# Optimization experiments

Hardware: AMD Instinct MI355X
Metric: run time of the kernel (lower is better)

Reference implementation:

```python
import jax, jax.numpy as jnp
import numpy as np


def setup_inputs() -> dict:
    key = jax.random.key(0)
    ks = jax.random.split(key, 9)
    N_POI, N_TIME, D = 10000, 48, 500
    S, L = 2048, 4096  # state_len (cur), seq_len (his)
    return {
        "his": jax.random.randint(ks[0], (L,), 0, N_POI, dtype=jnp.int32),
        "cur": jax.random.randint(ks[1], (S,), 0, N_POI, dtype=jnp.int32),
        "his_t": jax.random.randint(ks[2], (L,), 0, N_TIME, dtype=jnp.int32),
        "cur_t": jax.random.randint(ks[3], (S,), 0, N_TIME, dtype=jnp.int32),
        "poi_distance_mat": jax.random.uniform(ks[4], (N_POI, N_POI), dtype=jnp.float32),
        "time_sim_mat": jax.random.uniform(ks[5], (N_TIME, N_TIME), dtype=jnp.float32),
        "user_emb": jax.random.normal(ks[6], (S, D), dtype=jnp.float32),
        "id_emb": jax.random.normal(ks[7], (L, D), dtype=jnp.float32),
        "socail_uid_emb": jax.random.normal(ks[8], (D,), dtype=jnp.float32),
        "w1_socail": jnp.float32(0.6),
        "w2_socail": jnp.float32(0.4),
    }


def reference(his, cur, his_t, cur_t, poi_distance_mat, time_sim_mat,
              user_emb, id_emb, socail_uid_emb, w1_socail, w2_socail):
    # Attn_loc: energies[i,j] = 1/dist[cur[i],his[j]] if nonzero else 1e-6
    d = poi_distance_mat[cur[:, None], his[None, :]]          # [S, L] gather
    nz = d != 0
    loc_energy = jnp.where(nz, 1.0 / jnp.where(nz, d, 1.0), 1e-6)
    attn_loc = jax.nn.softmax(loc_energy, axis=-1)

    # Attn_time: energies[i,j] = time_sim[cur_t[i], his_t[j]]
    time_energy = time_sim_mat[cur_t[:, None], his_t[None, :]]  # [S, L]
    attn_time = jax.nn.softmax(time_energy, axis=-1)

    # Attn_user ('dot'): w1 * <user_emb[i], id_emb[j]> + w2 * <socail, id_emb[j]>
    user_energy = (w1_socail * jnp.einsum('sd,ld->sl', user_emb, id_emb)
                   + w2_socail * (id_emb @ socail_uid_emb)[None, :])  # [S, L]
    attn_user = jax.nn.softmax(user_energy, axis=-1)

    return jnp.stack([attn_loc, attn_time, attn_user])  # [3, S, L]
```

## Files before the change

### kernel.cpp

```cpp
#include <hip/hip_runtime.h>
#include <math.h>

#define S_DIM 2048
#define L_DIM 4096
#define D_DIM 500
#define NPOI 10000
#define NTIME 48
#define EXP_SHIFT 40.0f

typedef __attribute__((ext_vector_type(8))) short short8;
typedef __attribute__((ext_vector_type(16))) float f32x16;

#define A_BYTES 4194304
#define PLANE_BYTES 12582912
#define LDSBUF 49152

__device__ __forceinline__ float wave_max(float v) {
#pragma unroll
  for (int o = 32; o > 0; o >>= 1) v = fmaxf(v, __shfl_down(v, o, 64));
  return v;
}
__device__ __forceinline__ float wave_sum(float v) {
#pragma unroll
  for (int o = 32; o > 0; o >>= 1) v += __shfl_down(v, o, 64);
  return v;
}
__device__ __forceinline__ float half_sum(float v) {
#pragma unroll
  for (int o = 16; o > 0; o >>= 1) v += __shfl_xor(v, o, 64);
  return v;
}
__device__ __forceinline__ short f2bf(float x) {
  union { float f; unsigned u; } v;
  v.f = x;
  const unsigned r = v.u + 0x7fffu + ((v.u >> 16) & 1u);
  return (short)(r >> 16);
}
__device__ __forceinline__ float bf2f(short h) {
  union { unsigned u; float f; } v;
  v.u = ((unsigned)(unsigned short)h) << 16;
  return v.f;
}

__global__ __launch_bounds__(256) void split_table_kernel(
    const float* __restrict__ U, const float* __restrict__ Id,
    const float* __restrict__ w1p, const float* __restrict__ soc,
    const float* __restrict__ w2p, const int* __restrict__ his_t,
    const float* __restrict__ T, short* __restrict__ planes,
    float* __restrict__ bias, float* __restrict__ P) {
  const int tid = threadIdx.x;
  if (blockIdx.x == gridDim.x - 1) {
    __shared__ int cnt[NTIME];
    __shared__ float Ts[NTIME * NTIME];
    if (tid < NTIME) cnt[tid] = 0;
    __syncthreads();
    for (int l = tid; l < L_DIM; l += 256) atomicAdd(&cnt[his_t[l]], 1);
    for (int i = tid; i < NTIME * NTIME; i += 256) Ts[i] = T[i];
    __syncthreads();
    if (tid < NTIME) {
      float m = -1e30f;
      for (int t = 0; t < NTIME; ++t) m = fmaxf(m, Ts[tid * NTIME + t]);
      float den = 0.f;
      for (int t = 0; t < NTIME; ++t)
        den += (float)cnt[t] * __expf(Ts[tid * NTIME + t] - m);
      const float inv = 1.0f / den;
      for (int t = 0; t < NTIME; ++t)
        P[tid * NTIME + t] = __expf(Ts[tid * NTIME + t] - m) * inv;
    }
    return;
  }
  const int chunk = blockIdx.x * 256 + tid;
  const int row = chunk >> 6;
  const int lq = chunk & 63;
  const bool isA = row < S_DIM;
  const float scale = isA ? w1p[0] : 1.0f;
  const float* src = isA ? (U + (size_t)row * D_DIM)
                         : (Id + (size_t)(row - S_DIM) * D_DIM);
  const int k0 = lq * 8;
  float dot = 0.f;
  short h[8], l[8];
#pragma unroll
  for (int e = 0; e < 8; ++e) {
    const int k = k0 + e;
    const float v = (k < D_DIM) ? src[k] : 0.0f;
    if (!isA && k < D_DIM) dot += v * soc[k];
    const float x = scale * v;
    const short hb = f2bf(x);
    h[e] = hb;
    l[e] = f2bf(x - bf2f(hb));
  }
  const int ks = lq >> 2, g = lq & 3;
  if (isA) {
    const int mb = row >> 8, rin = row & 255;
    const int gs = g ^ (rin & 3) ^ ((rin >> 2) & 3);
    char* base =
        (char*)planes + (size_t)(mb * 16 + ks) * 32768 + rin * 64 + gs * 16;
    *reinterpret_cast<int4*>(base) = *reinterpret_cast<const int4*>(h);
    *reinterpret_cast<int4*>(base + 16384) = *reinterpret_cast<const int4*>(l);
  } else {
    const int rb = row - S_DIM;
    const int nb = rb >> 7, rin = rb & 127;
    const int gs = g ^ (rin & 3) ^ ((rin >> 2) & 3);
    char* base = (char*)planes + A_BYTES + (size_t)(nb * 16 + ks) * 16384 +
                 rin * 64 + gs * 16;
    *reinterpret_cast<int4*>(base) = *reinterpret_cast<const int4*>(h);
    *reinterpret_cast<int4*>(base + 8192) = *reinterpret_cast<const int4*>(l);
    const float d = wave_sum(dot);
    if ((tid & 63) == 0) bias[rb] = w2p[0] * d;
  }
}

__global__ __launch_bounds__(512, 2) void user_gemm_mfma(
    const short* __restrict__ planes, const float* __restrict__ bias,
    float* __restrict__ part, float* __restrict__ outX) {
  __shared__ __attribute__((aligned(1024))) char lds[2 * LDSBUF];
  const int tid = threadIdx.x;
  const int lane = tid & 63;
  const int wid = tid >> 6;
  const int ob = (blockIdx.x & 7) * 32 + (blockIdx.x >> 3);
  const int nb = ob >> 3;
  const int mb = ob & 7;
  const int bm = mb * 256, bn = nb * 128;
  const char* gA = (const char*)planes + (size_t)mb * 16 * 32768;
  const char* gB = (const char*)planes + A_BYTES + (size_t)nb * 16 * 16384;
  const int wm = (wid >> 1) * 64;
  const int wn = (wid & 1) * 64;
  const int r32 = lane & 31;
  const int khl = lane >> 5;

  f32x16 acc[2][2] = {};

#define STAGE(ks_, buf_)                                                      \
  {                                                                           \
    const int _ks = (ks_);                                                    \
    char* _dst = lds + (buf_)*LDSBUF;                                         \
    _Pragma("unroll") for (int q = 0; q < 6; ++q) {                           \
      const int off = (q * 512 + tid) * 16;                                   \
      if (q < 4) {                                                            \
        __builtin_amdgcn_global_load_lds(                                     \
            (const __attribute__((address_space(1))) unsigned*)(gA +          \
                (size_t)_ks * 32768 + off),                                   \
            (__attribute__((address_space(3))) unsigned*)(_dst + off), 16, 0, \
            0);                                                               \
      } else {                                                                \
        __builtin_amdgcn_global_load_lds(                                     \
            (const __attribute__((address_space(1))) unsigned*)(gB +          \
                (size_t)_ks * 16384 + (off - 32768)),                         \
            (__attribute__((address_space(3))) unsigned*)(_dst + off), 16, 0, \
            0);                                                               \
      }                                                                       \
    }                                                                         \
  }

  STAGE(0, 0);
  __syncthreads();
  int buf = 0;
  for (int ks = 0; ks < 16; ++ks) {
    if (ks < 15) STAGE(ks + 1, buf ^ 1);
    const char* La = lds + buf * LDSBUF;
    const char* Lb = La + 32768;
#pragma unroll
    for (int s16 = 0; s16 < 2; ++s16) {
      short8 ah[2], al[2], bh[2], bl[2];
#pragma unroll
      for (int i = 0; i < 2; ++i) {
        const int ra = wm + i * 32 + r32;
        const int ga = ((s16 * 2 + khl) ^ (ra & 3) ^ ((ra >> 2) & 3)) * 16;
        ah[i] = *reinterpret_cast<const short8*>(La + ra * 64 + ga);
        al[i] = *reinterpret_cast<const short8*>(La + 16384 + ra * 64 + ga);
        const int rbb = wn + i * 32 + r32;
        const int gb = ((s16 * 2 + khl) ^ (rbb & 3) ^ ((rbb >> 2) & 3)) * 16;
        bh[i] = *reinterpret_cast<const short8*>(Lb + rbb * 64 + gb);
        bl[i] = *reinterpret_cast<const short8*>(Lb + 8192 + rbb * 64 + gb);
      }
#pragma unroll
      for (int i = 0; i < 2; ++i)
#pragma unroll
        for (int j = 0; j < 2; ++j) {
          acc[i][j] = __builtin_amdgcn_mfma_f32_32x32x16_bf16(
              ah[i], bh[j], acc[i][j], 0, 0, 0);
          acc[i][j] = __builtin_amdgcn_mfma_f32_32x32x16_bf16(
              ah[i], bl[j], acc[i][j], 0, 0, 0);
          acc[i][j] = __builtin_amdgcn_mfma_f32_32x32x16_bf16(
              al[i], bh[j], acc[i][j], 0, 0, 0);
        }
    }
    __syncthreads();
    buf ^= 1;
  }
#undef STAGE

  const int slot = nb * 2 + (wn >> 6);
  float bj[2];
#pragma unroll
  for (int j = 0; j < 2; ++j) bj[j] = bias[bn + wn + j * 32 + r32];
#pragma unroll
  for (int i = 0; i < 2; ++i) {
#pragma unroll
    for (int reg = 0; reg < 16; ++reg) {
      const int rowm = bm + wm + i * 32 + 4 * khl + (reg & 3) + 8 * (reg >> 2);
      const float e0 = __expf(acc[i][0][reg] + bj[0] - EXP_SHIFT);
      const float e1 = __expf(acc[i][1][reg] + bj[1] - EXP_SHIFT);
      outX[(size_t)rowm * L_DIM + bn + wn + r32] = e0;
      outX[(size_t)rowm * L_DIM + bn + wn + 32 + r32] = e1;
      const float hs = half_sum(e0 + e1);
      if (r32 == 0) part[(size_t)rowm * 64 + slot] = hs;
    }
  }
}

__global__ __launch_bounds__(256) void finalize_kernel(
    const int* __restrict__ cur, const int* __restrict__ his,
    const float* __restrict__ poi, const int* __restrict__ cur_t,
    const int* __restrict__ his_t, const float* __restrict__ P,
    const float* __restrict__ part, float* __restrict__ out_loc,
    float* __restrict__ out_time, float* __restrict__ out_user) {
  __shared__ __attribute__((aligned(16))) float rowbuf[NPOI];
  __shared__ float Prow[NTIME];
  __shared__ float redm[4];
  __shared__ float reds[4];
  __shared__ float sinv_sh;
  const int s = blockIdx.x;
  const int tid = threadIdx.x;
  if (tid < NTIME) Prow[tid] = P[cur_t[s] * NTIME + tid];
  if (tid < 64) {
    float p = part[(size_t)s * 64 + tid];
    p = wave_sum(p);
    if (tid == 0) sinv_sh = 1.0f / p;
  }
  const float* row = poi + (size_t)cur[s] * NPOI;
  for (int i = tid; i < NPOI / 4; i += 256)
    *reinterpret_cast<float4*>(&rowbuf[i * 4]) =
        *reinterpret_cast<const float4*>(row + i * 4);
  __syncthreads();
  const float sinv = sinv_sh;
  float* ou = out_user + (size_t)s * L_DIM;
#pragma unroll
  for (int q = 0; q < 4; ++q) {
    float4 x = *reinterpret_cast<const float4*>(&ou[(q * 256 + tid) * 4]);
    x.x *= sinv; x.y *= sinv; x.z *= sinv; x.w *= sinv;
    *reinterpret_cast<float4*>(&ou[(q * 256 + tid) * 4]) = x;
  }
  float v[16];
  float lmax = -1e30f;
#pragma unroll
  for (int j = 0; j < 16; ++j) {
    const int l = j * 256 + tid;
    const float d = rowbuf[his[l]];
    const float e = (d != 0.0f) ? (1.0f / d) : 1e-6f;
    v[j] = e;
    lmax = fmaxf(lmax, e);
  }
  lmax = wave_max(lmax);
  if ((tid & 63) == 0) redm[tid >> 6] = lmax;
  __syncthreads();
  const float m = fmaxf(fmaxf(redm[0], redm[1]), fmaxf(redm[2], redm[3]));
  float lsum = 0.f;
#pragma unroll
  for (int j = 0; j < 16; ++j) {
    v[j] = __expf(v[j] - m);
    lsum += v[j];
  }
  lsum = wave_sum(lsum);
  if ((tid & 63) == 0) reds[tid >> 6] = lsum;
  __syncthreads();
  const float inv = 1.0f / (reds[0] + reds[1] + reds[2] + reds[3]);
  float* ol = out_loc + (size_t)s * L_DIM;
  float* ot = out_time + (size_t)s * L_DIM;
#pragma unroll
  for (int j = 0; j < 16; ++j) {
    const int l = j * 256 + tid;
    ol[l] = v[j] * inv;
    ot[l] = Prow[his_t[l]];
  }
}

extern "C" void kernel_launch(void* const* d_in, const int* in_sizes, int n_in,
                              void* d_out, int out_size, void* d_ws,
                              size_t ws_size, hipStream_t stream) {
  const int* his = (const int*)d_in[0];
  const int* cur = (const int*)d_in[1];
  const int* his_t = (const int*)d_in[2];
  const int* cur_t = (const int*)d_in[3];
  const float* poi = (const float*)d_in[4];
  const float* tsim = (const float*)d_in[5];
  const float* uemb = (const float*)d_in[6];
  const float* idemb = (const float*)d_in[7];
  const float* soc = (const float*)d_in[8];
  const float* w1 = (const float*)d_in[9];
  const float* w2 = (const float*)d_in[10];

  float* out = (float*)d_out;
  float* out_loc = out;
  float* out_time = out + (size_t)S_DIM * L_DIM;
  float* out_user = out + 2 * (size_t)S_DIM * L_DIM;

  const size_t aux_bytes = (size_t)(L_DIM + NTIME * NTIME + S_DIM * 64) * 4;
  short* planes;
  float* bias;
  if (ws_size >= PLANE_BYTES + aux_bytes) {
    planes = (short*)d_ws;
    bias = (float*)((char*)d_ws + PLANE_BYTES);
  } else {
    planes = (short*)out_loc;
    bias = (float*)d_ws;
  }
  float* P = bias + L_DIM;
  float* part = P + NTIME * NTIME;

  hipLaunchKernelGGL(split_table_kernel,
                     dim3((S_DIM + L_DIM) * 64 / 256 + 1), dim3(256), 0,
                     stream, uemb, idemb, w1, soc, w2, his_t, tsim, planes,
                     bias, P);
  hipLaunchKernelGGL(user_gemm_mfma, dim3(256), dim3(512), 0, stream, planes,
                     bias, part, out_user);
  hipLaunchKernelGGL(finalize_kernel, dim3(S_DIM), dim3(256), 0, stream, cur,
                     his, poi, cur_t, his_t, P, part, out_loc, out_time,
                     out_user);
}
```

Baseline: 88.60 us.

## Store exp scores as packed bf16 intermediate and halve GEMM block tile

The GEMM kernel now writes its exponentiated user scores as packed bf16 pairs into a workspace buffer instead of fp32 into the output. The finalize kernel then unpacks them, normalizes and writes fp32, so the intermediate round-trip traffic is halved. The GEMM block tile also shrinks from 256x128 to 128x128 with 256 threads and 512 blocks, which uses less LDS and gives more blocks. This adds bf16 rounding of the unnormalized exponentials, and it only takes effect if the workspace is large enough.

```diff
diff --git a/kernel.cpp b/kernel.cpp
--- a/kernel.cpp
+++ b/kernel.cpp
@@ -13,7 +13,7 @@
 
 #define A_BYTES 4194304
 #define PLANE_BYTES 12582912
-#define LDSBUF 49152
+#define LDSBUF 32768
 
 __device__ __forceinline__ float wave_max(float v) {
 #pragma unroll
@@ -110,19 +110,22 @@
   }
 }
 
-__global__ __launch_bounds__(512, 2) void user_gemm_mfma(
+__global__ __launch_bounds__(256, 2) void user_gemm_mfma(
     const short* __restrict__ planes, const float* __restrict__ bias,
-    float* __restrict__ part, float* __restrict__ outX) {
+    float* __restrict__ part, unsigned* __restrict__ Xp,
+    float* __restrict__ outX) {
   __shared__ __attribute__((aligned(1024))) char lds[2 * LDSBUF];
   const int tid = threadIdx.x;
   const int lane = tid & 63;
   const int wid = tid >> 6;
-  const int ob = (blockIdx.x & 7) * 32 + (blockIdx.x >> 3);
-  const int nb = ob >> 3;
-  const int mb = ob & 7;
-  const int bm = mb * 256, bn = nb * 128;
-  const char* gA = (const char*)planes + (size_t)mb * 16 * 32768;
+  const int ob = (blockIdx.x & 7) * 64 + (blockIdx.x >> 3);
+  const int nb = ob >> 4;
+  const int mbb = ob & 15;
+  const int mb256 = mbb >> 1, hh = mbb & 1;
+  const int bm = mbb * 128, bn = nb * 128;
+  const char* gA = (const char*)planes + (size_t)mb256 * 16 * 32768;
   const char* gB = (const char*)planes + A_BYTES + (size_t)nb * 16 * 16384;
+  const int h8 = hh * 8192;
   const int wm = (wid >> 1) * 64;
   const int wn = (wid & 1) * 64;
   const int r32 = lane & 31;
@@ -132,23 +135,18 @@
 
 #define STAGE(ks_, buf_)                                                      \
   {                                                                           \
-    const int _ks = (ks_);                                                    \
+    const char* gAk = gA + (size_t)(ks_)*32768 + h8;                          \
+    const char* gBk = gB + (size_t)(ks_)*16384;                               \
     char* _dst = lds + (buf_)*LDSBUF;                                         \
-    _Pragma("unroll") for (int q = 0; q < 6; ++q) {                           \
-      const int off = (q * 512 + tid) * 16;                                   \
-      if (q < 4) {                                                            \
-        __builtin_amdgcn_global_load_lds(                                     \
-            (const __attribute__((address_space(1))) unsigned*)(gA +          \
-                (size_t)_ks * 32768 + off),                                   \
-            (__attribute__((address_space(3))) unsigned*)(_dst + off), 16, 0, \
-            0);                                                               \
-      } else {                                                                \
-        __builtin_amdgcn_global_load_lds(                                     \
-            (const __attribute__((address_space(1))) unsigned*)(gB +          \
-                (size_t)_ks * 16384 + (off - 32768)),                         \
-            (__attribute__((address_space(3))) unsigned*)(_dst + off), 16, 0, \
-            0);                                                               \
-      }                                                                       \
+    _Pragma("unroll") for (int q = 0; q < 8; ++q) {                           \
+      const int off = (q * 256 + tid) * 16;                                   \
+      const char* src = (q < 2)   ? (gAk + off)                               \
+                        : (q < 4) ? (gAk + off + 8192)                        \
+                                  : (gBk + off - 16384);                      \
+      __builtin_amdgcn_global_load_lds(                                       \
+          (const __attribute__((address_space(1))) unsigned*)src,             \
+          (__attribute__((address_space(3))) unsigned*)(_dst + off), 16, 0,   \
+          0);                                                                 \
     }                                                                         \
   }
 
@@ -158,7 +156,7 @@
   for (int ks = 0; ks < 16; ++ks) {
     if (ks < 15) STAGE(ks + 1, buf ^ 1);
     const char* La = lds + buf * LDSBUF;
-    const char* Lb = La + 32768;
+    const char* Lb = La + 16384;
 #pragma unroll
     for (int s16 = 0; s16 < 2; ++s16) {
       short8 ah[2], al[2], bh[2], bl[2];
@@ -167,7 +165,7 @@
         const int ra = wm + i * 32 + r32;
         const int ga = ((s16 * 2 + khl) ^ (ra & 3) ^ ((ra >> 2) & 3)) * 16;
         ah[i] = *reinterpret_cast<const short8*>(La + ra * 64 + ga);
-        al[i] = *reinterpret_cast<const short8*>(La + 16384 + ra * 64 + ga);
+        al[i] = *reinterpret_cast<const short8*>(La + 8192 + ra * 64 + ga);
         const int rbb = wn + i * 32 + r32;
         const int gb = ((s16 * 2 + khl) ^ (rbb & 3) ^ ((rbb >> 2) & 3)) * 16;
         bh[i] = *reinterpret_cast<const short8*>(Lb + rbb * 64 + gb);
@@ -201,8 +199,14 @@
       const int rowm = bm + wm + i * 32 + 4 * khl + (reg & 3) + 8 * (reg >> 2);
       const float e0 = __expf(acc[i][0][reg] + bj[0] - EXP_SHIFT);
       const float e1 = __expf(acc[i][1][reg] + bj[1] - EXP_SHIFT);
-      outX[(size_t)rowm * L_DIM + bn + wn + r32] = e0;
-      outX[(size_t)rowm * L_DIM + bn + wn + 32 + r32] = e1;
+      if (Xp) {
+        const unsigned u = ((unsigned)(unsigned short)f2bf(e0)) |
+                           (((unsigned)(unsigned short)f2bf(e1)) << 16);
+        Xp[(size_t)rowm * 2048 + ((bn + wn) >> 1) + r32] = u;
+      } else {
+        outX[(size_t)rowm * L_DIM + bn + wn + r32] = e0;
+        outX[(size_t)rowm * L_DIM + bn + wn + 32 + r32] = e1;
+      }
       const float hs = half_sum(e0 + e1);
       if (r32 == 0) part[(size_t)rowm * 64 + slot] = hs;
     }
@@ -213,8 +217,9 @@
     const int* __restrict__ cur, const int* __restrict__ his,
     const float* __restrict__ poi, const int* __restrict__ cur_t,
     const int* __restrict__ his_t, const float* __restrict__ P,
-    const float* __restrict__ part, float* __restrict__ out_loc,
-    float* __restrict__ out_time, float* __restrict__ out_user) {
+    const float* __restrict__ part, const unsigned* __restrict__ Xp,
+    float* __restrict__ out_loc, float* __restrict__ out_time,
+    float* __restrict__ out_user) {
   __shared__ __attribute__((aligned(16))) float rowbuf[NPOI];
   __shared__ float Prow[NTIME];
   __shared__ float redm[4];
@@ -235,11 +240,26 @@
   __syncthreads();
   const float sinv = sinv_sh;
   float* ou = out_user + (size_t)s * L_DIM;
-#pragma unroll
-  for (int q = 0; q < 4; ++q) {
-    float4 x = *reinterpret_cast<const float4*>(&ou[(q * 256 + tid) * 4]);
-    x.x *= sinv; x.y *= sinv; x.z *= sinv; x.w *= sinv;
-    *reinterpret_cast<float4*>(&ou[(q * 256 + tid) * 4]) = x;
+  if (Xp) {
+    const unsigned* xr = Xp + (size_t)s * 2048;
+#pragma unroll
+    for (int qq = 0; qq < 8; ++qq) {
+      const int q = qq * 256 + tid;
+      const unsigned u = xr[q];
+      const int g = (q >> 5) << 6, r = q & 31;
+      union { unsigned uu; float f; } a, b;
+      a.uu = u << 16;
+      b.uu = u & 0xffff0000u;
+      ou[g + r] = a.f * sinv;
+      ou[g + r + 32] = b.f * sinv;
+    }
+  } else {
+#pragma unroll
+    for (int q = 0; q < 4; ++q) {
+      float4 x = *reinterpret_cast<const float4*>(&ou[(q * 256 + tid) * 4]);
+      x.x *= sinv; x.y *= sinv; x.z *= sinv; x.w *= sinv;
+      *reinterpret_cast<float4*>(&ou[(q * 256 + tid) * 4]) = x;
+    }
   }
   float v[16];
   float lmax = -1e30f;
@@ -295,10 +315,16 @@
   float* out_time = out + (size_t)S_DIM * L_DIM;
   float* out_user = out + 2 * (size_t)S_DIM * L_DIM;
 
-  const size_t aux_bytes = (size_t)(L_DIM + NTIME * NTIME + S_DIM * 64) * 4;
+  const size_t base_aux = (size_t)(L_DIM + NTIME * NTIME + S_DIM * 64) * 4;
+  const size_t xp_bytes = (size_t)S_DIM * 2048 * 4;
   short* planes;
   float* bias;
-  if (ws_size >= PLANE_BYTES + aux_bytes) {
+  unsigned* Xp = nullptr;
+  if (ws_size >= PLANE_BYTES + base_aux + xp_bytes) {
+    planes = (short*)d_ws;
+    bias = (float*)((char*)d_ws + PLANE_BYTES);
+    Xp = (unsigned*)((char*)d_ws + PLANE_BYTES + base_aux);
+  } else if (ws_size >= PLANE_BYTES + base_aux) {
     planes = (short*)d_ws;
     bias = (float*)((char*)d_ws + PLANE_BYTES);
   } else {
@@ -312,9 +338,9 @@
                      dim3((S_DIM + L_DIM) * 64 / 256 + 1), dim3(256), 0,
                      stream, uemb, idemb, w1, soc, w2, his_t, tsim, planes,
                      bias, P);
-  hipLaunchKernelGGL(user_gemm_mfma, dim3(256), dim3(512), 0, stream, planes,
-                     bias, part, out_user);
+  hipLaunchKernelGGL(user_gemm_mfma, dim3(512), dim3(256), 0, stream, planes,
+                     bias, part, Xp, out_user);
   hipLaunchKernelGGL(finalize_kernel, dim3(S_DIM), dim3(256), 0, stream, cur,
-                     his, poi, cur_t, his_t, P, part, out_loc, out_time,
+                     his, poi, cur_t, his_t, P, part, Xp, out_loc, out_time,
                      out_user);
 }
```

Result: slower. 91.09 us (+2.8%).

## Fuse user GEMM with location/time softmax blocks in one heterogeneous launch

Applied to the files above, without the earlier changes.

Replaces the separate user GEMM and finalize kernels with one kernel. One in five blocks runs a smaller 128x128 MFMA GEMM tile, and the other blocks each compute one row of the location and time softmax. This overlaps the compute-bound GEMM with the memory-bound gather and softmax work on the same GPU, and raises the GEMM grid from 256 to 512 tiles. A light normalize kernel then rescales the user output rows. The trade-off is smaller GEMM tiles with less reuse, twice the partial sums, and an extra read and write of the user output. The old path is kept as a fallback when the workspace is too small.

```diff
diff --git a/kernel.cpp b/kernel.cpp
--- a/kernel.cpp
+++ b/kernel.cpp
@@ -13,7 +13,6 @@
 
 #define A_BYTES 4194304
 #define PLANE_BYTES 12582912
-#define LDSBUF 49152
 
 __device__ __forceinline__ float wave_max(float v) {
 #pragma unroll
@@ -110,10 +109,178 @@
   }
 }
 
-__global__ __launch_bounds__(512, 2) void user_gemm_mfma(
+__global__ __launch_bounds__(512, 2) void fused_gemm_loc(
+    const short* __restrict__ planes, const float* __restrict__ bias,
+    float* __restrict__ part, float* __restrict__ outX,
+    const int* __restrict__ cur, const int* __restrict__ his,
+    const float* __restrict__ poi, const int* __restrict__ cur_t,
+    const int* __restrict__ his_t, const float* __restrict__ P,
+    float* __restrict__ out_loc, float* __restrict__ out_time) {
+  __shared__ __attribute__((aligned(1024))) char lds[65536];
+  __shared__ float redm[8];
+  __shared__ float reds[8];
+  __shared__ float Prow[NTIME];
+  const int tid = threadIdx.x;
+  const int lane = tid & 63;
+  const int wid = tid >> 6;
+  const int gb = blockIdx.x;
+
+  if (gb % 5 == 0) {
+    const int gi = gb / 5;
+    const int nb = gi & 31, mbb = gi >> 5;
+    const int mb256 = mbb >> 1, hh = mbb & 1;
+    const int bm = mbb * 128, bn = nb * 128;
+    const char* gA =
+        (const char*)planes + (size_t)mb256 * 16 * 32768 + hh * 8192;
+    const char* gB = (const char*)planes + A_BYTES + (size_t)nb * 16 * 16384;
+    const int wm = (wid >> 2) * 64;
+    const int wn = (wid & 3) * 32;
+    const int r32 = lane & 31;
+    const int khl = lane >> 5;
+
+    f32x16 acc[2] = {};
+
+#define STAGE(ks_, buf_)                                                      \
+  {                                                                           \
+    const char* gAk = gA + (size_t)(ks_)*32768;                               \
+    const char* gBk = gB + (size_t)(ks_)*16384;                               \
+    char* _dst = lds + (buf_)*32768;                                          \
+    _Pragma("unroll") for (int q = 0; q < 4; ++q) {                           \
+      const int off = (q * 512 + tid) * 16;                                   \
+      const char* src = (q == 0)   ? (gAk + off)                              \
+                        : (q == 1) ? (gAk + off + 8192)                       \
+                                   : (gBk + (off - 16384));                   \
+      __builtin_amdgcn_global_load_lds(                                       \
+          (const __attribute__((address_space(1))) unsigned*)src,             \
+          (__attribute__((address_space(3))) unsigned*)(_dst + off), 16, 0,   \
+          0);                                                                 \
+    }                                                                         \
+  }
+
+    STAGE(0, 0);
+    __syncthreads();
+    int buf = 0;
+    for (int ks = 0; ks < 16; ++ks) {
+      if (ks < 15) STAGE(ks + 1, buf ^ 1);
+      const char* La = lds + buf * 32768;
+      const char* Lb = La + 16384;
+#pragma unroll
+      for (int s16 = 0; s16 < 2; ++s16) {
+        short8 ah[2], al[2], bh, bl;
+#pragma unroll
+        for (int i = 0; i < 2; ++i) {
+          const int ra = wm + i * 32 + r32;
+          const int ga = ((s16 * 2 + khl) ^ (ra & 3) ^ ((ra >> 2) & 3)) * 16;
+          ah[i] = *reinterpret_cast<const short8*>(La + ra * 64 + ga);
+          al[i] = *reinterpret_cast<const short8*>(La + 8192 + ra * 64 + ga);
+        }
+        const int rbb = wn + r32;
+        const int gbx = ((s16 * 2 + khl) ^ (rbb & 3) ^ ((rbb >> 2) & 3)) * 16;
+        bh = *reinterpret_cast<const short8*>(Lb + rbb * 64 + gbx);
+        bl = *reinterpret_cast<const short8*>(Lb + 8192 + rbb * 64 + gbx);
+#pragma unroll
+        for (int i = 0; i < 2; ++i) {
+          acc[i] =
+              __builtin_amdgcn_mfma_f32_32x32x16_bf16(ah[i], bh, acc[i], 0, 0, 0);
+          acc[i] =
+              __builtin_amdgcn_mfma_f32_32x32x16_bf16(ah[i], bl, acc[i], 0, 0, 0);
+          acc[i] =
+              __builtin_amdgcn_mfma_f32_32x32x16_bf16(al[i], bh, acc[i], 0, 0, 0);
+        }
+      }
+      __syncthreads();
+      buf ^= 1;
+    }
+#undef STAGE
+
+    const float bj = bias[bn + wn + r32];
+    const int slot = nb * 4 + (wid & 3);
+#pragma unroll
+    for (int i = 0; i < 2; ++i) {
+#pragma unroll
+      for (int reg = 0; reg < 16; ++reg) {
+        const int rowm =
+            bm + wm + i * 32 + 4 * khl + (reg & 3) + 8 * (reg >> 2);
+        const float e = __expf(acc[i][reg] + bj - EXP_SHIFT);
+        outX[(size_t)rowm * L_DIM + bn + wn + r32] = e;
+        const float hs = half_sum(e);
+        if (r32 == 0) part[(size_t)rowm * 128 + slot] = hs;
+      }
+    }
+  } else {
+    const int s = (gb / 5) * 4 + (gb % 5) - 1;
+    float* rowbuf = (float*)lds;
+    if (tid < NTIME) Prow[tid] = P[cur_t[s] * NTIME + tid];
+    const float* row = poi + (size_t)cur[s] * NPOI;
+    for (int i = tid; i < NPOI / 4; i += 512)
+      reinterpret_cast<float4*>(rowbuf)[i] =
+          reinterpret_cast<const float4*>(row)[i];
+    __syncthreads();
+    float v[8];
+    float lmax = -1e30f;
+#pragma unroll
+    for (int j = 0; j < 8; ++j) {
+      const int l = j * 512 + tid;
+      const float d = rowbuf[his[l]];
+      const float e = (d != 0.0f) ? (1.0f / d) : 1e-6f;
+      v[j] = e;
+      lmax = fmaxf(lmax, e);
+    }
+    lmax = wave_max(lmax);
+    if (lane == 0) redm[wid] = lmax;
+    __syncthreads();
+    float m = redm[0];
+#pragma unroll
+    for (int w = 1; w < 8; ++w) m = fmaxf(m, redm[w]);
+    float lsum = 0.f;
+#pragma unroll
+    for (int j = 0; j < 8; ++j) {
+      v[j] = __expf(v[j] - m);
+      lsum += v[j];
+    }
+    lsum = wave_sum(lsum);
+    if (lane == 0) reds[wid] = lsum;
+    __syncthreads();
+    float tot = reds[0];
+#pragma unroll
+    for (int w = 1; w < 8; ++w) tot += reds[w];
+    const float inv = 1.0f / tot;
+    float* ol = out_loc + (size_t)s * L_DIM;
+    float* ot = out_time + (size_t)s * L_DIM;
+#pragma unroll
+    for (int j = 0; j < 8; ++j) {
+      const int l = j * 512 + tid;
+      ol[l] = v[j] * inv;
+      ot[l] = Prow[his_t[l]];
+    }
+  }
+}
+
+__global__ __launch_bounds__(256) void normalize_kernel(
+    const float* __restrict__ part, float* __restrict__ outU) {
+  __shared__ float sinv_sh;
+  const int s = blockIdx.x;
+  const int tid = threadIdx.x;
+  if (tid < 64) {
+    float p = part[(size_t)s * 128 + tid] + part[(size_t)s * 128 + 64 + tid];
+    p = wave_sum(p);
+    if (tid == 0) sinv_sh = 1.0f / p;
+  }
+  __syncthreads();
+  const float sinv = sinv_sh;
+  float* ou = outU + (size_t)s * L_DIM;
+#pragma unroll
+  for (int q = 0; q < 4; ++q) {
+    float4 x = *reinterpret_cast<const float4*>(&ou[(q * 256 + tid) * 4]);
+    x.x *= sinv; x.y *= sinv; x.z *= sinv; x.w *= sinv;
+    *reinterpret_cast<float4*>(&ou[(q * 256 + tid) * 4]) = x;
+  }
+}
+
+__global__ __launch_bounds__(512, 2) void user_gemm_fb(
     const short* __restrict__ planes, const float* __restrict__ bias,
     float* __restrict__ part, float* __restrict__ outX) {
-  __shared__ __attribute__((aligned(1024))) char lds[2 * LDSBUF];
+  __shared__ __attribute__((aligned(1024))) char lds[2 * 49152];
   const int tid = threadIdx.x;
   const int lane = tid & 63;
   const int wid = tid >> 6;
@@ -127,13 +294,11 @@
   const int wn = (wid & 1) * 64;
   const int r32 = lane & 31;
   const int khl = lane >> 5;
-
   f32x16 acc[2][2] = {};
-
 #define STAGE(ks_, buf_)                                                      \
   {                                                                           \
     const int _ks = (ks_);                                                    \
-    char* _dst = lds + (buf_)*LDSBUF;                                         \
+    char* _dst = lds + (buf_)*49152;                                          \
     _Pragma("unroll") for (int q = 0; q < 6; ++q) {                           \
       const int off = (q * 512 + tid) * 16;                                   \
       if (q < 4) {                                                            \
@@ -151,13 +316,12 @@
       }                                                                       \
     }                                                                         \
   }
-
   STAGE(0, 0);
   __syncthreads();
   int buf = 0;
   for (int ks = 0; ks < 16; ++ks) {
     if (ks < 15) STAGE(ks + 1, buf ^ 1);
-    const char* La = lds + buf * LDSBUF;
+    const char* La = lds + buf * 49152;
     const char* Lb = La + 32768;
 #pragma unroll
     for (int s16 = 0; s16 < 2; ++s16) {
@@ -169,9 +333,9 @@
         ah[i] = *reinterpret_cast<const short8*>(La + ra * 64 + ga);
         al[i] = *reinterpret_cast<const short8*>(La + 16384 + ra * 64 + ga);
         const int rbb = wn + i * 32 + r32;
-        const int gb = ((s16 * 2 + khl) ^ (rbb & 3) ^ ((rbb >> 2) & 3)) * 16;
-        bh[i] = *reinterpret_cast<const short8*>(Lb + rbb * 64 + gb);
-        bl[i] = *reinterpret_cast<const short8*>(Lb + 8192 + rbb * 64 + gb);
+        const int gbx = ((s16 * 2 + khl) ^ (rbb & 3) ^ ((rbb >> 2) & 3)) * 16;
+        bh[i] = *reinterpret_cast<const short8*>(Lb + rbb * 64 + gbx);
+        bl[i] = *reinterpret_cast<const short8*>(Lb + 8192 + rbb * 64 + gbx);
       }
 #pragma unroll
       for (int i = 0; i < 2; ++i)
@@ -189,7 +353,6 @@
     buf ^= 1;
   }
 #undef STAGE
-
   const int slot = nb * 2 + (wn >> 6);
   float bj[2];
 #pragma unroll
@@ -209,7 +372,7 @@
   }
 }
 
-__global__ __launch_bounds__(256) void finalize_kernel(
+__global__ __launch_bounds__(256) void finalize_fb(
     const int* __restrict__ cur, const int* __restrict__ his,
     const float* __restrict__ poi, const int* __restrict__ cur_t,
     const int* __restrict__ his_t, const float* __restrict__ P,
@@ -295,26 +458,43 @@
   float* out_time = out + (size_t)S_DIM * L_DIM;
   float* out_user = out + 2 * (size_t)S_DIM * L_DIM;
 
-  const size_t aux_bytes = (size_t)(L_DIM + NTIME * NTIME + S_DIM * 64) * 4;
-  short* planes;
-  float* bias;
-  if (ws_size >= PLANE_BYTES + aux_bytes) {
-    planes = (short*)d_ws;
-    bias = (float*)((char*)d_ws + PLANE_BYTES);
+  const size_t fused_aux = (size_t)(L_DIM + NTIME * NTIME + S_DIM * 128) * 4;
+  const size_t fb_aux = (size_t)(L_DIM + NTIME * NTIME + S_DIM * 64) * 4;
+
+  if (ws_size >= PLANE_BYTES + fused_aux) {
+    short* planes = (short*)d_ws;
+    float* bias = (float*)((char*)d_ws + PLANE_BYTES);
+    float* P = bias + L_DIM;
+    float* part = P + NTIME * NTIME;
+    hipLaunchKernelGGL(split_table_kernel,
+                       dim3((S_DIM + L_DIM) * 64 / 256 + 1), dim3(256), 0,
+                       stream, uemb, idemb, w1, soc, w2, his_t, tsim, planes,
+                       bias, P);
+    hipLaunchKernelGGL(fused_gemm_loc, dim3(2560), dim3(512), 0, stream,
+                       planes, bias, part, out_user, cur, his, poi, cur_t,
+                       his_t, P, out_loc, out_time);
+    hipLaunchKernelGGL(normalize_kernel, dim3(S_DIM), dim3(256), 0, stream,
+                       part, out_user);
   } else {
-    planes = (short*)out_loc;
-    bias = (float*)d_ws;
-  }
-  float* P = bias + L_DIM;
-  float* part = P + NTIME * NTIME;
-
-  hipLaunchKernelGGL(split_table_kernel,
-                     dim3((S_DIM + L_DIM) * 64 / 256 + 1), dim3(256), 0,
-                     stream, uemb, idemb, w1, soc, w2, his_t, tsim, planes,
-                     bias, P);
-  hipLaunchKernelGGL(user_gemm_mfma, dim3(256), dim3(512), 0, stream, planes,
-                     bias, part, out_user);
-  hipLaunchKernelGGL(finalize_kernel, dim3(S_DIM), dim3(256), 0, stream, cur,
-                     his, poi, cur_t, his_t, P, part, out_loc, out_time,
-                     out_user);
-}
+    short* planes;
+    float* bias;
+    if (ws_size >= PLANE_BYTES + fb_aux) {
+      planes = (short*)d_ws;
+      bias = (float*)((char*)d_ws + PLANE_BYTES);
+    } else {
+      planes = (short*)out_loc;
+      bias = (float*)d_ws;
+    }
+    float* P = bias + L_DIM;
+    float* part = P + NTIME * NTIME;
+    hipLaunchKernelGGL(split_table_kernel,
+                       dim3((S_DIM + L_DIM) * 64 / 256 + 1), dim3(256), 0,
+                       stream, uemb, idemb, w1, soc, w2, his_t, tsim, planes,
+                       bias, P);
+    hipLaunchKernelGGL(user_gemm_fb, dim3(256), dim3(512), 0, stream, planes,
+                       bias, part, out_user);
+    hipLaunchKernelGGL(finalize_fb, dim3(S_DIM), dim3(256), 0, stream, cur,
+                       his, poi, cur_t, his_t, P, part, out_loc, out_time,
+                       out_user);
+  }
+}
```

Measured after the change: 99.98 us. +12.9%, slower.

## Store unnormalized user exponentials as packed bf16 in the first half of each output row

Applied to the files above, without the earlier changes.

The GEMM epilogue packs each pair of exp values into bf16 and writes them as 32-bit words into the first half of each output row, so it writes half as many bytes as before. The finalize kernel reads all packed words into registers before any write, unpacks them, scales by the inverse row sum and writes the full fp32 row in place. This cuts write and read traffic on the intermediate, but the output keeps only bf16 precision, which risks a tolerance failure. The in-place overwrite stays correct only because every packed word for the row is loaded before the first store.

```diff
diff --git a/kernel.cpp b/kernel.cpp
--- a/kernel.cpp
+++ b/kernel.cpp
@@ -112,7 +112,7 @@
 
 __global__ __launch_bounds__(512, 2) void user_gemm_mfma(
     const short* __restrict__ planes, const float* __restrict__ bias,
-    float* __restrict__ part, float* __restrict__ outX) {
+    float* __restrict__ part, float* __restrict__ outU) {
   __shared__ __attribute__((aligned(1024))) char lds[2 * LDSBUF];
   const int tid = threadIdx.x;
   const int lane = tid & 63;
@@ -190,7 +190,8 @@
   }
 #undef STAGE
 
-  const int slot = nb * 2 + (wn >> 6);
+  const int slot = ((bn + wn) >> 1) + r32;
+  const int pslot = nb * 2 + (wn >> 6);
   float bj[2];
 #pragma unroll
   for (int j = 0; j < 2; ++j) bj[j] = bias[bn + wn + j * 32 + r32];
@@ -201,10 +202,11 @@
       const int rowm = bm + wm + i * 32 + 4 * khl + (reg & 3) + 8 * (reg >> 2);
       const float e0 = __expf(acc[i][0][reg] + bj[0] - EXP_SHIFT);
       const float e1 = __expf(acc[i][1][reg] + bj[1] - EXP_SHIFT);
-      outX[(size_t)rowm * L_DIM + bn + wn + r32] = e0;
-      outX[(size_t)rowm * L_DIM + bn + wn + 32 + r32] = e1;
+      const unsigned u = ((unsigned)(unsigned short)f2bf(e0)) |
+                         (((unsigned)(unsigned short)f2bf(e1)) << 16);
+      reinterpret_cast<unsigned*>(outU + (size_t)rowm * L_DIM)[slot] = u;
       const float hs = half_sum(e0 + e1);
-      if (r32 == 0) part[(size_t)rowm * 64 + slot] = hs;
+      if (r32 == 0) part[(size_t)rowm * 64 + pslot] = hs;
     }
   }
 }
@@ -228,18 +230,28 @@
     p = wave_sum(p);
     if (tid == 0) sinv_sh = 1.0f / p;
   }
+  float* ou = out_user + (size_t)s * L_DIM;
+  unsigned xv[8];
+  {
+    const unsigned* xr = reinterpret_cast<const unsigned*>(ou);
+#pragma unroll
+    for (int qq = 0; qq < 8; ++qq) xv[qq] = xr[qq * 256 + tid];
+  }
   const float* row = poi + (size_t)cur[s] * NPOI;
   for (int i = tid; i < NPOI / 4; i += 256)
     *reinterpret_cast<float4*>(&rowbuf[i * 4]) =
         *reinterpret_cast<const float4*>(row + i * 4);
   __syncthreads();
   const float sinv = sinv_sh;
-  float* ou = out_user + (size_t)s * L_DIM;
-#pragma unroll
-  for (int q = 0; q < 4; ++q) {
-    float4 x = *reinterpret_cast<const float4*>(&ou[(q * 256 + tid) * 4]);
-    x.x *= sinv; x.y *= sinv; x.z *= sinv; x.w *= sinv;
-    *reinterpret_cast<float4*>(&ou[(q * 256 + tid) * 4]) = x;
+#pragma unroll
+  for (int qq = 0; qq < 8; ++qq) {
+    const int q = qq * 256 + tid;
+    const int g = (q >> 5) << 6, r = q & 31;
+    union { unsigned uu; float f; } a, b;
+    a.uu = xv[qq] << 16;
+    b.uu = xv[qq] & 0xffff0000u;
+    ou[g + r] = a.f * sinv;
+    ou[g + r + 32] = b.f * sinv;
   }
   float v[16];
   float lmax = -1e30f;
```

After: 87.56 us. About the same (-1.2%).
